# Optimization experiments

Hardware: AMD Instinct MI355X
Metric: run time of the kernel (lower is better)

The kernel has to match this reference:

```python
import jax, jax.numpy as jnp
import numpy as np

HEADS = 20
HEAD_DIM = 64  # 1280 / 20
IP_SCALE = 1.0


def _split_heads(x, B):
    # [B, S, H*D] -> [B, H, S, D]
    return x.reshape(B, -1, HEADS, HEAD_DIM).transpose(0, 2, 1, 3)


def _merge_heads(x, B):
    # [B, H, S, D] -> [B, S, H*D]
    return x.transpose(0, 2, 1, 3).reshape(B, -1, HEADS * HEAD_DIM)


def _sdpa(q, k, v):
    # q:[B,H,Sq,D] k,v:[B,H,Sk,D]
    scale = 1.0 / jnp.sqrt(jnp.asarray(HEAD_DIM, q.dtype))
    scores = jnp.einsum('bhqd,bhkd->bhqk', q, k) * scale
    probs = jax.nn.softmax(scores, axis=-1)
    return jnp.einsum('bhqk,bhkd->bhqd', probs, v)


def setup_inputs() -> dict:
    key = jax.random.key(0)
    ks = jax.random.split(key, 10)
    B, S, D = 8, 4096, 1280
    Ctx, Cdim = 77, 2048
    Adim = 768
    inp = {
        'hidden_states': jax.random.normal(ks[0], (B, S, D), jnp.float32),
        'encoder_hidden_states': jax.random.normal(ks[1], (B, Ctx, Cdim), jnp.float32),
        'adapter_embeds': jax.random.normal(ks[2], (B, 1, Adim), jnp.float32),
        'Wq': jax.random.normal(ks[3], (D, D), jnp.float32) * 0.02,
        'Wk': jax.random.normal(ks[4], (Cdim, D), jnp.float32) * 0.02,
        'Wv': jax.random.normal(ks[5], (Cdim, D), jnp.float32) * 0.02,
        'Wk_adapter': jax.random.normal(ks[6], (Adim, D), jnp.float32) * 0.02,
        'Wv_adapter': jax.random.normal(ks[7], (Adim, D), jnp.float32) * 0.02,
        'Wo': jax.random.normal(ks[8], (D, D), jnp.float32) * 0.02,
        'bo': jnp.zeros((D,), jnp.float32),
    }
    return inp


def reference(hidden_states, encoder_hidden_states, adapter_embeds,
              Wq, Wk, Wv, Wk_adapter, Wv_adapter, Wo, bo):
    B = hidden_states.shape[0]

    # base cross-attention projections
    q = _split_heads(hidden_states @ Wq, B)                 # [B,H,S,D]
    k = _split_heads(encoder_hidden_states @ Wk, B)         # [B,H,77,D]
    v = _split_heads(encoder_hidden_states @ Wv, B)
    out = _merge_heads(_sdpa(q, k, v), B)                   # [B,S,H*D]

    # IP-adapter branch: single-token K/V, shares the same query
    k_ip = _split_heads(adapter_embeds @ Wk_adapter, B)     # [B,H,1,D]
    v_ip = _split_heads(adapter_embeds @ Wv_adapter, B)
    out_ip = _merge_heads(_sdpa(q, k_ip, v_ip), B)

    merged = out + IP_SCALE * out_ip
    return merged @ Wo + bo
```

## Files before the change

### kernel.cpp

```cpp
#include <hip/hip_runtime.h>
#include <hip/hip_bf16.h>
#include <cstdint>
#include <cstddef>

typedef __hip_bfloat16 bf16_t;
typedef __attribute__((ext_vector_type(8))) __bf16 bf16x8;
typedef __attribute__((ext_vector_type(4))) float f32x4;

__device__ __forceinline__ void gld_lds16(const void* g, void* l) {
    __builtin_amdgcn_global_load_lds(
        (const __attribute__((address_space(1))) void*)(g),
        (__attribute__((address_space(3))) void*)(l), 16, 0, 0);
}

__global__ void k_cast(const float* __restrict__ in, bf16_t* __restrict__ out, long n) {
    long i = ((long)blockIdx.x * blockDim.x + threadIdx.x) * 4;
    if (i >= n) return;
    float4 v = *(const float4*)(in + i);
    out[i + 0] = __float2bfloat16(v.x);
    out[i + 1] = __float2bfloat16(v.y);
    out[i + 2] = __float2bfloat16(v.z);
    out[i + 3] = __float2bfloat16(v.w);
}

__global__ void k_cast_pad(const float* __restrict__ in, bf16_t* __restrict__ out,
                           int rows_in, int rows_out, int cols) {
    long i = ((long)blockIdx.x * blockDim.x + threadIdx.x) * 4;
    long n = (long)rows_out * cols;
    if (i >= n) return;
    int r = (int)(i / cols);
    if (r < rows_in) {
        float4 v = *(const float4*)(in + i);
        out[i + 0] = __float2bfloat16(v.x);
        out[i + 1] = __float2bfloat16(v.y);
        out[i + 2] = __float2bfloat16(v.z);
        out[i + 3] = __float2bfloat16(v.w);
    } else {
        bf16_t z = __float2bfloat16(0.f);
        out[i + 0] = z; out[i + 1] = z; out[i + 2] = z; out[i + 3] = z;
    }
}

__global__ void k_transpose_cast(const float* __restrict__ in, bf16_t* __restrict__ out,
                                 int R, int C) {
    __shared__ float tile[32][33];
    int bx = blockIdx.x * 32;
    int by = blockIdx.y * 32;
    int tx = threadIdx.x & 31, ty = threadIdx.x >> 5;
    #pragma unroll
    for (int j = 0; j < 32; j += 8)
        tile[ty + j][tx] = in[(size_t)(by + ty + j) * C + bx + tx];
    __syncthreads();
    #pragma unroll
    for (int j = 0; j < 32; j += 8)
        out[(size_t)(bx + ty + j) * R + by + tx] = __float2bfloat16(tile[tx][ty + j]);
}

__global__ void k_adapter(const float* __restrict__ ae, const float* __restrict__ Wva,
                          float* __restrict__ vip) {
    int g = blockIdx.x * 256 + threadIdx.x;
    int b = g / 1280, n = g % 1280;
    const float* a = ae + b * 768;
    float acc = 0.f;
    for (int k = 0; k < 768; ++k) acc += a[k] * Wva[(size_t)k * 1280 + n];
    vip[g] = acc;
}

template <bool OUT_BF16, bool ADD_BIAS, bool SWZ>
__global__ __launch_bounds__(256, 2) void k_gemm_bt(
    const bf16_t* __restrict__ A, const bf16_t* __restrict__ Bt,
    void* __restrict__ Cv, const float* __restrict__ bias, int M, int N, int K,
    int snt, int mtx) {
    __shared__ __align__(16) bf16_t As[128 * 32];
    __shared__ __align__(16) bf16_t Bs[128 * 32];
    const int tid = threadIdx.x;
    int m0, n0;
    if constexpr (SWZ) {
        int id = blockIdx.x;
        int xcd = id & 7, j = id >> 3;
        m0 = (xcd * mtx + j / snt) * 128;
        n0 = (j % snt) * 128;
    } else {
        m0 = blockIdx.y * 128;
        n0 = blockIdx.x * 128;
    }
    const int wave = tid >> 6, lane = tid & 63;
    const int wm = (wave >> 1) * 64, wn = (wave & 1) * 64;
    const int quad = lane >> 4, l16 = lane & 15;

    f32x4 acc[4][4] = {};

    const int c0 = tid, c1 = tid + 256;
    const int r0 = c0 >> 2, o0 = (c0 & 3) * 8;
    const int r1 = c1 >> 2, o1 = (c1 & 3) * 8;
    const bf16_t* a0 = A + (size_t)(m0 + r0) * K + o0;
    const bf16_t* a1 = A + (size_t)(m0 + r1) * K + o1;
    const bf16_t* b0 = Bt + (size_t)(n0 + r0) * K + o0;
    const bf16_t* b1 = Bt + (size_t)(n0 + r1) * K + o1;

    for (int k0 = 0; k0 < K; k0 += 32) {
        __syncthreads();
        gld_lds16(a0 + k0, As + c0 * 8);
        gld_lds16(a1 + k0, As + c1 * 8);
        gld_lds16(b0 + k0, Bs + c0 * 8);
        gld_lds16(b1 + k0, Bs + c1 * 8);
        __syncthreads();
        bf16x8 af[4], bfv[4];
        #pragma unroll
        for (int t = 0; t < 4; ++t) {
            af[t]  = *(const bf16x8*)(As + (wm + t * 16 + l16) * 32 + quad * 8);
            bfv[t] = *(const bf16x8*)(Bs + (wn + t * 16 + l16) * 32 + quad * 8);
        }
        #pragma unroll
        for (int mt = 0; mt < 4; ++mt)
            #pragma unroll
            for (int nt = 0; nt < 4; ++nt)
                acc[mt][nt] = __builtin_amdgcn_mfma_f32_16x16x32_bf16(af[mt], bfv[nt], acc[mt][nt], 0, 0, 0);
    }

    if constexpr (OUT_BF16) {
        bf16_t* C = (bf16_t*)Cv;
        #pragma unroll
        for (int mt = 0; mt < 4; ++mt)
            #pragma unroll
            for (int rg = 0; rg < 4; ++rg) {
                int row = m0 + wm + mt * 16 + quad * 4 + rg;
                #pragma unroll
                for (int nt = 0; nt < 4; ++nt) {
                    int col = n0 + wn + nt * 16 + l16;
                    C[(size_t)row * N + col] = __float2bfloat16(acc[mt][nt][rg]);
                }
            }
    } else {
        float* C = (float*)Cv;
        float bv[4];
        #pragma unroll
        for (int nt = 0; nt < 4; ++nt)
            bv[nt] = ADD_BIAS ? bias[n0 + wn + nt * 16 + l16] : 0.f;
        #pragma unroll
        for (int mt = 0; mt < 4; ++mt)
            #pragma unroll
            for (int rg = 0; rg < 4; ++rg) {
                int row = m0 + wm + mt * 16 + quad * 4 + rg;
                #pragma unroll
                for (int nt = 0; nt < 4; ++nt) {
                    int col = n0 + wn + nt * 16 + l16;
                    C[(size_t)row * N + col] = acc[mt][nt][rg] + bv[nt];
                }
            }
    }
}

__global__ __launch_bounds__(256, 2) void k_attn(
    const bf16_t* __restrict__ Q, const bf16_t* __restrict__ Kc,
    const bf16_t* __restrict__ Vc, const float* __restrict__ vip,
    bf16_t* __restrict__ Mrg) {
    __shared__ __align__(16) bf16_t Qs[128 * 64];
    __shared__ __align__(16) bf16_t Ks[96 * 64];
    __shared__ __align__(16) bf16_t Vt[64 * 96];
    __shared__ __align__(16) bf16_t Ps[128 * 96];
    const int tid = threadIdx.x;
    const int qb = blockIdx.x, h = blockIdx.y, b = blockIdx.z;
    const int wave = tid >> 6, lane = tid & 63;
    const int quad = lane >> 4, l16 = lane & 15;

    const bf16_t* Qg = Q + ((size_t)(b * 4096 + qb * 128)) * 1280 + h * 64;
    #pragma unroll
    for (int j = 0; j < 4; ++j) {
        int c = tid + j * 256;
        int r = c >> 3, o = (c & 7) * 8;
        gld_lds16(Qg + (size_t)r * 1280 + o, Qs + c * 8);
    }
    bf16_t z = __float2bfloat16(0.f);
    for (int i = 77 * 64 + tid; i < 96 * 64; i += 256) Ks[i] = z;
    for (int i = tid; i < 64 * 19; i += 256) {
        int d = i / 19, kk = 77 + i % 19;
        Vt[d * 96 + kk] = z;
    }
    for (int c = tid; c < 616; c += 256) {
        int r = c >> 3, o = (c & 7) * 8;
        size_t gi = ((size_t)(b * 77 + r)) * 1280 + h * 64 + o;
        int4 kv = *(const int4*)(Kc + gi);
        *(int4*)(Ks + r * 64 + o) = kv;
        int4 vv = *(const int4*)(Vc + gi);
        const bf16_t* ve = (const bf16_t*)&vv;
        #pragma unroll
        for (int j = 0; j < 8; ++j) Vt[(o + j) * 96 + r] = ve[j];
    }
    __syncthreads();

    f32x4 sacc[2][6] = {};
    #pragma unroll
    for (int ks = 0; ks < 2; ++ks) {
        bf16x8 aq[2], bk[6];
        #pragma unroll
        for (int mt = 0; mt < 2; ++mt)
            aq[mt] = *(const bf16x8*)(Qs + (wave * 32 + mt * 16 + l16) * 64 + ks * 32 + quad * 8);
        #pragma unroll
        for (int nt = 0; nt < 6; ++nt)
            bk[nt] = *(const bf16x8*)(Ks + (nt * 16 + l16) * 64 + ks * 32 + quad * 8);
        #pragma unroll
        for (int mt = 0; mt < 2; ++mt)
            #pragma unroll
            for (int nt = 0; nt < 6; ++nt)
                sacc[mt][nt] = __builtin_amdgcn_mfma_f32_16x16x32_bf16(aq[mt], bk[nt], sacc[mt][nt], 0, 0, 0);
    }
    #pragma unroll
    for (int mt = 0; mt < 2; ++mt)
        #pragma unroll
        for (int nt = 0; nt < 6; ++nt)
            #pragma unroll
            for (int rg = 0; rg < 4; ++rg) {
                int row = wave * 32 + mt * 16 + quad * 4 + rg;
                int col = nt * 16 + l16;
                Ps[row * 96 + col] = __float2bfloat16(sacc[mt][nt][rg] * 0.125f);
            }
    __syncthreads();

    {
        int row = tid >> 1, half = tid & 1;
        int cbeg = half ? 39 : 0, cend = half ? 77 : 39;
        bf16_t* prow = Ps + row * 96;
        float mx = -1e30f;
        for (int c = cbeg; c < cend; ++c) mx = fmaxf(mx, __bfloat162float(prow[c]));
        mx = fmaxf(mx, __shfl_xor(mx, 1));
        float sm = 0.f;
        for (int c = cbeg; c < cend; ++c) sm += __expf(__bfloat162float(prow[c]) - mx);
        sm += __shfl_xor(sm, 1);
        float inv = 1.f / sm;
        for (int c = cbeg; c < cend; ++c)
            prow[c] = __float2bfloat16(__expf(__bfloat162float(prow[c]) - mx) * inv);
    }
    __syncthreads();

    f32x4 oacc[2][4] = {};
    #pragma unroll
    for (int ks = 0; ks < 3; ++ks) {
        bf16x8 ap[2], bv[4];
        #pragma unroll
        for (int mt = 0; mt < 2; ++mt)
            ap[mt] = *(const bf16x8*)(Ps + (wave * 32 + mt * 16 + l16) * 96 + ks * 32 + quad * 8);
        #pragma unroll
        for (int nt = 0; nt < 4; ++nt)
            bv[nt] = *(const bf16x8*)(Vt + (nt * 16 + l16) * 96 + ks * 32 + quad * 8);
        #pragma unroll
        for (int mt = 0; mt < 2; ++mt)
            #pragma unroll
            for (int nt = 0; nt < 4; ++nt)
                oacc[mt][nt] = __builtin_amdgcn_mfma_f32_16x16x32_bf16(ap[mt], bv[nt], oacc[mt][nt], 0, 0, 0);
    }
    #pragma unroll
    for (int nt = 0; nt < 4; ++nt) {
        int col = nt * 16 + l16;
        float add = vip[b * 1280 + h * 64 + col];
        #pragma unroll
        for (int mt = 0; mt < 2; ++mt)
            #pragma unroll
            for (int rg = 0; rg < 4; ++rg) {
                int row = wave * 32 + mt * 16 + quad * 4 + rg;
                Mrg[((size_t)(b * 4096 + qb * 128 + row)) * 1280 + h * 64 + col] =
                    __float2bfloat16(oacc[mt][nt][rg] + add);
            }
    }
}

extern "C" void kernel_launch(void* const* d_in, const int* in_sizes, int n_in,
                              void* d_out, int out_size, void* d_ws, size_t ws_size,
                              hipStream_t stream) {
    (void)in_sizes; (void)n_in; (void)out_size; (void)ws_size;
    const float* hs  = (const float*)d_in[0];
    const float* enc = (const float*)d_in[1];
    const float* ae  = (const float*)d_in[2];
    const float* Wq  = (const float*)d_in[3];
    const float* Wk  = (const float*)d_in[4];
    const float* Wv  = (const float*)d_in[5];
    const float* Wva = (const float*)d_in[7];
    const float* Wo  = (const float*)d_in[8];
    const float* bo  = (const float*)d_in[9];
    float* out = (float*)d_out;

    char* ws = (char*)d_ws;
    size_t off = 0;
    auto alloc = [&](size_t bytes) -> void* {
        void* p = ws + off;
        off += (bytes + 255) & ~(size_t)255;
        return p;
    };
    bf16_t* Xb  = (bf16_t*)alloc((size_t)32768 * 1280 * 2);
    bf16_t* Qb  = (bf16_t*)alloc((size_t)32768 * 1280 * 2);
    bf16_t* Mrg = (bf16_t*)alloc((size_t)32768 * 1280 * 2);
    bf16_t* Eb  = (bf16_t*)alloc((size_t)640 * 2048 * 2);
    bf16_t* WqT = (bf16_t*)alloc((size_t)1280 * 1280 * 2);
    bf16_t* WkT = (bf16_t*)alloc((size_t)1280 * 2048 * 2);
    bf16_t* WvT = (bf16_t*)alloc((size_t)1280 * 2048 * 2);
    bf16_t* WoT = (bf16_t*)alloc((size_t)1280 * 1280 * 2);
    bf16_t* Kc  = (bf16_t*)alloc((size_t)640 * 1280 * 2);
    bf16_t* Vc  = (bf16_t*)alloc((size_t)640 * 1280 * 2);
    float*  vip = (float*)alloc((size_t)8 * 1280 * 4);

    k_cast<<<40960, 256, 0, stream>>>(hs, Xb, (long)32768 * 1280);
    k_cast_pad<<<1280, 256, 0, stream>>>(enc, Eb, 616, 640, 2048);
    k_transpose_cast<<<dim3(40, 40), 256, 0, stream>>>(Wq, WqT, 1280, 1280);
    k_transpose_cast<<<dim3(40, 64), 256, 0, stream>>>(Wk, WkT, 2048, 1280);
    k_transpose_cast<<<dim3(40, 64), 256, 0, stream>>>(Wv, WvT, 2048, 1280);
    k_transpose_cast<<<dim3(40, 40), 256, 0, stream>>>(Wo, WoT, 1280, 1280);
    k_adapter<<<40, 256, 0, stream>>>(ae, Wva, vip);

    k_gemm_bt<true, false, true><<<2560, 256, 0, stream>>>(Xb, WqT, Qb, nullptr, 32768, 1280, 1280, 10, 32);
    k_gemm_bt<true, false, false><<<dim3(10, 5), 256, 0, stream>>>(Eb, WkT, Kc, nullptr, 640, 1280, 2048, 0, 0);
    k_gemm_bt<true, false, false><<<dim3(10, 5), 256, 0, stream>>>(Eb, WvT, Vc, nullptr, 640, 1280, 2048, 0, 0);

    k_attn<<<dim3(32, 20, 8), 256, 0, stream>>>(Qb, Kc, Vc, vip, Mrg);

    k_gemm_bt<false, true, true><<<2560, 256, 0, stream>>>(Mrg, WoT, out, bo, 32768, 1280, 1280, 10, 32);
}
```

Before: 864.5 us.

## Add 256x256 pipelined GEMM, fuse K/V and transpose launches, stage attention stores

```diff
diff --git a/kernel.cpp b/kernel.cpp
--- a/kernel.cpp
+++ b/kernel.cpp
@@ -41,9 +41,12 @@
     }
 }
 
-__global__ void k_transpose_cast(const float* __restrict__ in, bf16_t* __restrict__ out,
-                                 int R, int C) {
+__global__ void k_transpose_cast2(const float* __restrict__ in0, bf16_t* __restrict__ out0,
+                                  const float* __restrict__ in1, bf16_t* __restrict__ out1,
+                                  int R, int C) {
     __shared__ float tile[32][33];
+    const float* in = blockIdx.z ? in1 : in0;
+    bf16_t* out = blockIdx.z ? out1 : out0;
     int bx = blockIdx.x * 32;
     int by = blockIdx.y * 32;
     int tx = threadIdx.x & 31, ty = threadIdx.x >> 5;
@@ -151,10 +154,173 @@
     }
 }
 
+template <bool OUT_BF16, bool ADD_BIAS, int KC>
+__global__ __launch_bounds__(512, 2) void k_gemm256(
+    const bf16_t* __restrict__ A, const bf16_t* __restrict__ Bt,
+    void* __restrict__ Cv, const float* __restrict__ bias,
+    int N, int snt, int mtx) {
+    __shared__ __align__(16) bf16_t As[2][256 * 64];
+    __shared__ __align__(16) bf16_t Bs[2][256 * 64];
+    const int tid = threadIdx.x;
+    const int id = blockIdx.x;
+    const int xcd = id & 7, jb = id >> 3;
+    const int m0 = (xcd * mtx + jb / snt) * 256;
+    const int n0 = (jb % snt) * 256;
+    const int wave = tid >> 6, lane = tid & 63;
+    const int wm = wave >> 2, wn = wave & 3;
+    const int quad = lane >> 4, l16 = lane & 15;
+
+    const int lr0 = tid >> 3;
+    const int cst = ((tid & 7) * 8) ^ ((lr0 & 7) * 8);
+    const bf16_t* pA0 = A + (size_t)(m0 + lr0) * KC + cst;
+    const bf16_t* pA1 = pA0 + (size_t)128 * KC;
+    const bf16_t* pB0 = Bt + (size_t)(n0 + ((lr0 >> 5) << 6) + (lr0 & 31)) * KC + cst;
+    const bf16_t* pB1 = pB0 + (size_t)128 * KC;
+    const int eA0 = tid * 8, eA1 = 4096 + tid * 8;
+
+    const int xorc = (l16 & 7) * 8;
+    const int c0x = (quad * 8) ^ xorc;
+    const int c1x = (32 + quad * 8) ^ xorc;
+    const int arow = (wm * 64 + l16) * 64;
+    const int brow = (wn * 32 + l16) * 64;
+
+    f32x4 acc[8][4] = {};
+    bf16x8 afA[4][2], afB[4][2], bf0[2][2], bf1[2][2];
+
+#define SA0_(WB, T) do { size_t ko_ = (size_t)(T) * 64; \
+    gld_lds16(pA0 + ko_, &As[WB][eA0]); gld_lds16(pA1 + ko_, &As[WB][eA1]); } while (0)
+#define SA1_(WB, T) do { size_t ko_ = (size_t)(T) * 64 + (size_t)64 * KC; \
+    gld_lds16(pA0 + ko_, &As[WB][8192 + eA0]); gld_lds16(pA1 + ko_, &As[WB][8192 + eA1]); } while (0)
+#define SB0_(WB, T) do { size_t ko_ = (size_t)(T) * 64; \
+    gld_lds16(pB0 + ko_, &Bs[WB][eA0]); gld_lds16(pB1 + ko_, &Bs[WB][eA1]); } while (0)
+#define SB1_(WB, T) do { size_t ko_ = (size_t)(T) * 64 + (size_t)32 * KC; \
+    gld_lds16(pB0 + ko_, &Bs[WB][8192 + eA0]); gld_lds16(pB1 + ko_, &Bs[WB][8192 + eA1]); } while (0)
+#define RD_AFA(RB_) do { _Pragma("unroll") for (int mt = 0; mt < 4; ++mt) { \
+    const bf16_t* p_ = &As[RB_][arow + mt * 1024]; \
+    afA[mt][0] = *(const bf16x8*)(p_ + c0x); afA[mt][1] = *(const bf16x8*)(p_ + c1x); } } while (0)
+#define RD_AFB(RB_) do { _Pragma("unroll") for (int mt = 0; mt < 4; ++mt) { \
+    const bf16_t* p_ = &As[RB_][8192 + arow + mt * 1024]; \
+    afB[mt][0] = *(const bf16x8*)(p_ + c0x); afB[mt][1] = *(const bf16x8*)(p_ + c1x); } } while (0)
+#define RD_BF0(RB_) do { _Pragma("unroll") for (int nt = 0; nt < 2; ++nt) { \
+    const bf16_t* p_ = &Bs[RB_][brow + nt * 1024]; \
+    bf0[nt][0] = *(const bf16x8*)(p_ + c0x); bf0[nt][1] = *(const bf16x8*)(p_ + c1x); } } while (0)
+#define RD_BF1(RB_) do { _Pragma("unroll") for (int nt = 0; nt < 2; ++nt) { \
+    const bf16_t* p_ = &Bs[RB_][8192 + brow + nt * 1024]; \
+    bf1[nt][0] = *(const bf16x8*)(p_ + c0x); bf1[nt][1] = *(const bf16x8*)(p_ + c1x); } } while (0)
+#define MMA_(AF, BF, MB, NB) do { _Pragma("unroll") \
+    for (int mt = 0; mt < 4; ++mt) _Pragma("unroll") \
+    for (int nt = 0; nt < 2; ++nt) _Pragma("unroll") \
+    for (int ks = 0; ks < 2; ++ks) \
+      acc[(MB) + mt][(NB) + nt] = __builtin_amdgcn_mfma_f32_16x16x32_bf16( \
+          AF[mt][ks], BF[nt][ks], acc[(MB) + mt][(NB) + nt], 0, 0, 0); } while (0)
+#define BAR_ asm volatile("s_barrier" ::: "memory")
+#define VM_(n) asm volatile("s_waitcnt vmcnt(" #n ")" ::: "memory")
+#define LG_(n) do { asm volatile("s_waitcnt lgkmcnt(" #n ")" ::: "memory"); \
+    __builtin_amdgcn_sched_barrier(0); } while (0)
+#define P1_ __builtin_amdgcn_s_setprio(1)
+#define P0_ __builtin_amdgcn_s_setprio(0)
+
+#define TILE_(T, RB) do { \
+    RD_BF1(RB); SA1_((RB) ^ 1, (T) + 1); VM_(8); BAR_; \
+    LG_(4); P1_; MMA_(afA, bf0, 0, 0); P0_; BAR_; \
+    RD_AFB(RB); SA0_(RB, (T) + 2); VM_(8); BAR_; \
+    LG_(8); P1_; MMA_(afA, bf1, 0, 2); P0_; BAR_; \
+    RD_AFA((RB) ^ 1); SB0_(RB, (T) + 2); VM_(8); BAR_; \
+    LG_(8); P1_; MMA_(afB, bf0, 4, 0); P0_; BAR_; \
+    RD_BF0((RB) ^ 1); SB1_(RB, (T) + 2); VM_(8); BAR_; \
+    P1_; MMA_(afB, bf1, 4, 2); P0_; BAR_; \
+  } while (0)
+
+    const int NT = KC >> 6;
+
+    SA0_(0, 0); SB0_(0, 0); SB1_(0, 0); SA1_(0, 0);
+    SA0_(1, 1); SB0_(1, 1); SB1_(1, 1);
+    VM_(8);
+    BAR_;
+    RD_AFA(0); RD_BF0(0);
+
+    #pragma unroll 1
+    for (int t = 0; t < NT - 2; t += 2) {
+        TILE_(t, 0);
+        TILE_(t + 1, 1);
+    }
+
+    RD_BF1(0); SA1_(1, NT - 1); VM_(8); BAR_;
+    LG_(4); P1_; MMA_(afA, bf0, 0, 0); P0_; BAR_;
+    RD_AFB(0); VM_(6); BAR_;
+    LG_(8); P1_; MMA_(afA, bf1, 0, 2); P0_; BAR_;
+    RD_AFA(1); VM_(4); BAR_;
+    LG_(8); P1_; MMA_(afB, bf0, 4, 0); P0_; BAR_;
+    RD_BF0(1); VM_(2); BAR_;
+    P1_; MMA_(afB, bf1, 4, 2); P0_; BAR_;
+    RD_BF1(1); VM_(0); BAR_;
+    RD_AFB(1);
+    LG_(12); P1_; MMA_(afA, bf0, 0, 0); P0_;
+    LG_(8);  P1_; MMA_(afA, bf1, 0, 2); P0_;
+    LG_(0);  P1_; MMA_(afB, bf0, 4, 0); P0_;
+    P1_; MMA_(afB, bf1, 4, 2); P0_;
+
+#undef SA0_
+#undef SA1_
+#undef SB0_
+#undef SB1_
+#undef RD_AFA
+#undef RD_AFB
+#undef RD_BF0
+#undef RD_BF1
+#undef MMA_
+#undef BAR_
+#undef VM_
+#undef LG_
+#undef P1_
+#undef P0_
+#undef TILE_
+
+    if constexpr (OUT_BF16) {
+        bf16_t* C = (bf16_t*)Cv;
+        __syncthreads();
+        bf16_t* eb = wm ? (bf16_t*)Bs : (bf16_t*)As;
+        #pragma unroll
+        for (int mt = 0; mt < 8; ++mt)
+            #pragma unroll
+            for (int rg = 0; rg < 4; ++rg) {
+                int rr = (mt >> 2) * 64 + (mt & 3) * 16 + quad * 4 + rg;
+                #pragma unroll
+                for (int nt = 0; nt < 4; ++nt)
+                    eb[rr * 256 + wn * 64 + nt * 16 + l16] = __float2bfloat16(acc[mt][nt][rg]);
+            }
+        __syncthreads();
+        #pragma unroll
+        for (int pass = 0; pass < 16; ++pass) {
+            const bf16_t* sb = (pass < 8) ? (const bf16_t*)As : (const bf16_t*)Bs;
+            int r = pass * 16 + (tid >> 5);
+            int cc = (tid & 31) * 8;
+            *(int4*)(&C[(size_t)(m0 + r) * N + n0 + cc]) =
+                *(const int4*)(sb + (r & 127) * 256 + cc);
+        }
+    } else {
+        float* C = (float*)Cv;
+        float bv[4];
+        #pragma unroll
+        for (int nt = 0; nt < 4; ++nt)
+            bv[nt] = ADD_BIAS ? bias[n0 + wn * 64 + nt * 16 + l16] : 0.f;
+        #pragma unroll
+        for (int mt = 0; mt < 8; ++mt)
+            #pragma unroll
+            for (int rg = 0; rg < 4; ++rg) {
+                int row = m0 + wm * 128 + (mt >> 2) * 64 + (mt & 3) * 16 + quad * 4 + rg;
+                #pragma unroll
+                for (int nt = 0; nt < 4; ++nt) {
+                    int col = n0 + wn * 64 + nt * 16 + l16;
+                    C[(size_t)row * N + col] = acc[mt][nt][rg] + bv[nt];
+                }
+            }
+    }
+}
+
 __global__ __launch_bounds__(256, 2) void k_attn(
-    const bf16_t* __restrict__ Q, const bf16_t* __restrict__ Kc,
-    const bf16_t* __restrict__ Vc, const float* __restrict__ vip,
-    bf16_t* __restrict__ Mrg) {
+    const bf16_t* __restrict__ Q, const bf16_t* __restrict__ KV,
+    const float* __restrict__ vip, bf16_t* __restrict__ Mrg) {
     __shared__ __align__(16) bf16_t Qs[128 * 64];
     __shared__ __align__(16) bf16_t Ks[96 * 64];
     __shared__ __align__(16) bf16_t Vt[64 * 96];
@@ -179,10 +345,10 @@
     }
     for (int c = tid; c < 616; c += 256) {
         int r = c >> 3, o = (c & 7) * 8;
-        size_t gi = ((size_t)(b * 77 + r)) * 1280 + h * 64 + o;
-        int4 kv = *(const int4*)(Kc + gi);
+        size_t gi = ((size_t)(b * 77 + r)) * 2560 + h * 64 + o;
+        int4 kv = *(const int4*)(KV + gi);
         *(int4*)(Ks + r * 64 + o) = kv;
-        int4 vv = *(const int4*)(Vc + gi);
+        int4 vv = *(const int4*)(KV + gi + 1280);
         const bf16_t* ve = (const bf16_t*)&vv;
         #pragma unroll
         for (int j = 0; j < 8; ++j) Vt[(o + j) * 96 + r] = ve[j];
@@ -249,6 +415,7 @@
             for (int nt = 0; nt < 4; ++nt)
                 oacc[mt][nt] = __builtin_amdgcn_mfma_f32_16x16x32_bf16(ap[mt], bv[nt], oacc[mt][nt], 0, 0, 0);
     }
+    __syncthreads();
     #pragma unroll
     for (int nt = 0; nt < 4; ++nt) {
         int col = nt * 16 + l16;
@@ -258,9 +425,16 @@
             #pragma unroll
             for (int rg = 0; rg < 4; ++rg) {
                 int row = wave * 32 + mt * 16 + quad * 4 + rg;
-                Mrg[((size_t)(b * 4096 + qb * 128 + row)) * 1280 + h * 64 + col] =
-                    __float2bfloat16(oacc[mt][nt][rg] + add);
-            }
+                Ps[row * 64 + col] = __float2bfloat16(oacc[mt][nt][rg] + add);
+            }
+    }
+    __syncthreads();
+    #pragma unroll
+    for (int pass = 0; pass < 4; ++pass) {
+        int r = pass * 32 + (tid >> 3);
+        int cc = (tid & 7) * 8;
+        *(int4*)(Mrg + ((size_t)(b * 4096 + qb * 128 + r)) * 1280 + h * 64 + cc) =
+            *(const int4*)(Ps + r * 64 + cc);
     }
 }
 
@@ -286,31 +460,26 @@
         off += (bytes + 255) & ~(size_t)255;
         return p;
     };
-    bf16_t* Xb  = (bf16_t*)alloc((size_t)32768 * 1280 * 2);
-    bf16_t* Qb  = (bf16_t*)alloc((size_t)32768 * 1280 * 2);
-    bf16_t* Mrg = (bf16_t*)alloc((size_t)32768 * 1280 * 2);
-    bf16_t* Eb  = (bf16_t*)alloc((size_t)640 * 2048 * 2);
-    bf16_t* WqT = (bf16_t*)alloc((size_t)1280 * 1280 * 2);
-    bf16_t* WkT = (bf16_t*)alloc((size_t)1280 * 2048 * 2);
-    bf16_t* WvT = (bf16_t*)alloc((size_t)1280 * 2048 * 2);
-    bf16_t* WoT = (bf16_t*)alloc((size_t)1280 * 1280 * 2);
-    bf16_t* Kc  = (bf16_t*)alloc((size_t)640 * 1280 * 2);
-    bf16_t* Vc  = (bf16_t*)alloc((size_t)640 * 1280 * 2);
-    float*  vip = (float*)alloc((size_t)8 * 1280 * 4);
+    bf16_t* Xb   = (bf16_t*)alloc((size_t)32768 * 1280 * 2);
+    bf16_t* Qb   = (bf16_t*)alloc((size_t)32768 * 1280 * 2);
+    bf16_t* Mrg  = (bf16_t*)alloc((size_t)32768 * 1280 * 2);
+    bf16_t* Eb   = (bf16_t*)alloc((size_t)640 * 2048 * 2);
+    bf16_t* WqT  = (bf16_t*)alloc((size_t)1280 * 1280 * 2);
+    bf16_t* WkvT = (bf16_t*)alloc((size_t)2560 * 2048 * 2);
+    bf16_t* WoT  = (bf16_t*)alloc((size_t)1280 * 1280 * 2);
+    bf16_t* KVc  = (bf16_t*)alloc((size_t)640 * 2560 * 2);
+    float*  vip  = (float*)alloc((size_t)8 * 1280 * 4);
 
     k_cast<<<40960, 256, 0, stream>>>(hs, Xb, (long)32768 * 1280);
     k_cast_pad<<<1280, 256, 0, stream>>>(enc, Eb, 616, 640, 2048);
-    k_transpose_cast<<<dim3(40, 40), 256, 0, stream>>>(Wq, WqT, 1280, 1280);
-    k_transpose_cast<<<dim3(40, 64), 256, 0, stream>>>(Wk, WkT, 2048, 1280);
-    k_transpose_cast<<<dim3(40, 64), 256, 0, stream>>>(Wv, WvT, 2048, 1280);
-    k_transpose_cast<<<dim3(40, 40), 256, 0, stream>>>(Wo, WoT, 1280, 1280);
+    k_transpose_cast2<<<dim3(40, 40, 2), 256, 0, stream>>>(Wq, WqT, Wo, WoT, 1280, 1280);
+    k_transpose_cast2<<<dim3(40, 64, 2), 256, 0, stream>>>(Wk, WkvT, Wv, WkvT + (size_t)1280 * 2048, 2048, 1280);
     k_adapter<<<40, 256, 0, stream>>>(ae, Wva, vip);
 
-    k_gemm_bt<true, false, true><<<2560, 256, 0, stream>>>(Xb, WqT, Qb, nullptr, 32768, 1280, 1280, 10, 32);
-    k_gemm_bt<true, false, false><<<dim3(10, 5), 256, 0, stream>>>(Eb, WkT, Kc, nullptr, 640, 1280, 2048, 0, 0);
-    k_gemm_bt<true, false, false><<<dim3(10, 5), 256, 0, stream>>>(Eb, WvT, Vc, nullptr, 640, 1280, 2048, 0, 0);
-
-    k_attn<<<dim3(32, 20, 8), 256, 0, stream>>>(Qb, Kc, Vc, vip, Mrg);
-
-    k_gemm_bt<false, true, true><<<2560, 256, 0, stream>>>(Mrg, WoT, out, bo, 32768, 1280, 1280, 10, 32);
-}
+    k_gemm256<true, false, 1280><<<640, 512, 0, stream>>>(Xb, WqT, Qb, nullptr, 1280, 5, 16);
+    k_gemm_bt<true, false, false><<<dim3(20, 5), 256, 0, stream>>>(Eb, WkvT, KVc, nullptr, 640, 2560, 2048, 0, 0);
+
+    k_attn<<<dim3(32, 20, 8), 256, 0, stream>>>(Qb, KVc, vip, Mrg);
+
+    k_gemm256<false, true, 1280><<<640, 512, 0, stream>>>(Mrg, WoT, out, bo, 1280, 5, 16);
+}
```

Measured after the change: 830.8 us. -3.9%, faster.
